# Optimization experiments

Hardware: AMD Instinct MI355X
Metric: run time of the kernel (lower is better)

The kernel has to match this reference:

```python
import jax, jax.numpy as jnp
import numpy as np

D = 1024      # model_dim
H = 16        # num_heads
DH = D // H   # depth per head
F = 4096      # ffn_dim
B, L = 4, 2048
LN_EPS = 1e-5


def layer_norm(x, g, b):
    mu = jnp.mean(x, axis=-1, keepdims=True)
    var = jnp.var(x, axis=-1, keepdims=True)
    return (x - mu) * jax.lax.rsqrt(var + LN_EPS) * g + b


def setup_inputs() -> dict:
    key = jax.random.key(0)
    ks = jax.random.split(key, 12)
    s = 0.02
    return {
        "inputs": jax.random.normal(ks[0], (B, L, D), jnp.float32),
        "Wq": jax.random.normal(ks[1], (D, D), jnp.float32) * s,
        "Wk": jax.random.normal(ks[2], (D, D), jnp.float32) * s,
        "Wv": jax.random.normal(ks[3], (D, D), jnp.float32) * s,
        "Wo": jax.random.normal(ks[4], (D, D), jnp.float32) * s,
        "W1": jax.random.normal(ks[5], (F, D), jnp.float32) * s,
        "b1": jnp.zeros((F,), jnp.float32),
        "W2": jax.random.normal(ks[6], (D, F), jnp.float32) * s,
        "b2": jnp.zeros((D,), jnp.float32),
        "ln_g": jnp.ones((D,), jnp.float32),
        "ln_b": jnp.zeros((D,), jnp.float32),
    }


def reference(inputs, Wq, Wk, Wv, Wo, W1, b1, W2, b2, ln_g, ln_b):
    # --- MultiHeadAttention (faithful to source, incl. the bug where
    # ScaledDotProductAttention returns v, not attention @ v) ---
    scale = DH ** -0.5
    q = (inputs @ Wq.T) * scale            # [B,L,D], scaled before head split
    k = inputs @ Wk.T                      # [B,L,D]
    v = inputs @ Wv.T                      # [B,L,D]
    # only the LAST head's attention scores survive the python loop
    qH = q[..., (H - 1) * DH:]             # [B,L,DH]
    kH = k[..., (H - 1) * DH:]             # [B,L,DH]
    attn = jax.nn.softmax(jnp.einsum('bqd,bkd->bqk', qH, kH), axis=-1) / H
    # combine_heads(split_heads(v)) == v, so context = Wo applied to v
    context = v @ Wo.T                     # [B,L,D]; dropout(p=0) is identity

    # --- PositionalWiseFeedForward: conv1d(kernel=1) == pointwise linear ---
    h = jax.nn.relu(context @ W1.T + b1)   # [B,L,F]
    ffn = h @ W2.T + b2                    # [B,L,D]
    out = layer_norm(context + ffn, ln_g, ln_b)
    return out, attn
```

## Files before the change

### kernel.cpp

```cpp
#include <hip/hip_runtime.h>
#include <hip/hip_bf16.h>
#include <stdint.h>

#define D_ 1024
#define H_ 16
#define DH_ 64
#define F_ 4096
#define B_ 4
#define L_ 2048
#define MTOK 8192

typedef __attribute__((ext_vector_type(8))) short bf16x8;
typedef __attribute__((ext_vector_type(4))) float f32x4;

__device__ __forceinline__ short f2bf(float f) {
  uint32_t u = __float_as_uint(f);
  uint32_t r = (u + 0x7FFFu + ((u >> 16) & 1u)) >> 16;
  return (short)(uint16_t)r;
}
__device__ __forceinline__ float bf2f(short s) {
  return __uint_as_float(((uint32_t)(uint16_t)s) << 16);
}

__device__ __forceinline__ void gload_lds16(const short* g, short* l) {
  __builtin_amdgcn_global_load_lds(
      (const __attribute__((address_space(1))) void*)g,
      (__attribute__((address_space(3))) void*)l,
      16, 0, 0);
}

__global__ void __launch_bounds__(256) convert_bf16(
    const float* __restrict__ src, short* __restrict__ dst, long n, float scale) {
  long i = ((long)blockIdx.x * 256 + threadIdx.x) * 4;
  long stride = (long)gridDim.x * 1024;
  for (; i < n; i += stride) {
    float4 f = *(const float4*)(src + i);
    short4 o;
    o.x = f2bf(f.x * scale);
    o.y = f2bf(f.y * scale);
    o.z = f2bf(f.z * scale);
    o.w = f2bf(f.w * scale);
    *(short4*)(dst + i) = o;
  }
}

__global__ void __launch_bounds__(256) convert_weights(
    const float* __restrict__ Wq, const float* __restrict__ Wk,
    const float* __restrict__ Wv, const float* __restrict__ Wo,
    const float* __restrict__ W1, const float* __restrict__ W2,
    short* __restrict__ wqk, short* __restrict__ wv, short* __restrict__ wo,
    short* __restrict__ w1, short* __restrict__ w2) {
  long i = ((long)blockIdx.x * 256 + threadIdx.x) * 4;
  const float* src; short* dst; long off; float scale = 1.0f;
  if (i < 65536L)            { src = Wq + 960L * 1024; dst = wqk;        off = i;            scale = 0.125f; }
  else if (i < 131072L)      { src = Wk + 960L * 1024; dst = wqk + 65536; off = i - 65536L;  }
  else if (i < 1179648L)     { src = Wv; dst = wv; off = i - 131072L;   }
  else if (i < 2228224L)     { src = Wo; dst = wo; off = i - 1179648L;  }
  else if (i < 6422528L)     { src = W1; dst = w1; off = i - 2228224L;  }
  else                       { src = W2; dst = w2; off = i - 6422528L;  }
  float4 f = *(const float4*)(src + off);
  short4 o4;
  o4.x = f2bf(f.x * scale); o4.y = f2bf(f.y * scale);
  o4.z = f2bf(f.z * scale); o4.w = f2bf(f.w * scale);
  *(short4*)(dst + off) = o4;
}

#define BAR   __builtin_amdgcn_s_barrier()
#define PRIO1 __builtin_amdgcn_s_setprio(1)
#define PRIO0 __builtin_amdgcn_s_setprio(0)
#define LGKM0 asm volatile("s_waitcnt lgkmcnt(0)" ::: "memory")

#define RD_A(mh_, par_) do {                                                  \
  const short* bp = lds + (par_) * BUF + wm * ASLOT;                          \
  _Pragma("unroll")                                                           \
  for (int m2 = 0; m2 < MH; m2++) {                                           \
    const int r = ((mh_) * MH + m2) * 16 + l15;                               \
    _Pragma("unroll")                                                         \
    for (int ks = 0; ks < 2; ks++)                                            \
      aF[mh_][m2][ks] =                                                       \
          *(const bf16x8*)(bp + r * 64 + (((ks * 4 + l4) ^ (r & 7)) << 3));   \
  } } while (0)

#define RD_B(nh_, par_) do {                                                  \
  const short* bp = lds + (par_) * BUF + BM * 64 + (wn >> 1) * 8192;          \
  _Pragma("unroll")                                                           \
  for (int n2 = 0; n2 < 2; n2++) {                                            \
    const int r = (wn & 1) * 64 + ((nh_) * 2 + n2) * 16 + l15;                \
    _Pragma("unroll")                                                         \
    for (int ks = 0; ks < 2; ks++)                                            \
      bF[nh_][n2][ks] =                                                       \
          *(const bf16x8*)(bp + r * 64 + (((ks * 4 + l4) ^ (r & 7)) << 3));   \
  } } while (0)

#define QUAD(mh_, nh_) do {                                                   \
  _Pragma("unroll")                                                           \
  for (int ks = 0; ks < 2; ks++)                                              \
    _Pragma("unroll")                                                         \
    for (int m2 = 0; m2 < MH; m2++)                                           \
      _Pragma("unroll")                                                       \
      for (int n2 = 0; n2 < 2; n2++)                                          \
        acc[(mh_) * MH + m2][(nh_) * 2 + n2] =                                \
            __builtin_amdgcn_mfma_f32_16x16x32_bf16(                          \
                aF[mh_][m2][ks], bF[nh_][n2][ks],                             \
                acc[(mh_) * MH + m2][(nh_) * 2 + n2], 0, 0, 0);               \
} while (0)

#define ITER2(g_, par_, SN, SPP, GK) do {                                     \
                                                                 \
  RD_A(0, par_); RD_B(0, par_); RD_B(1, par_);                                \
  if (SN) stA((g_) + 1, 1, (par_) ^ 1);                                       \
  LGKM0;                                                                      \
  PRIO1; QUAD(0, 0); QUAD(0, 1); PRIO0;                                       \
  BAR;              \
                                                                 \
  RD_A(1, par_);                                                              \
  if (SPP) { stB((g_) + 2, 0, par_); stB((g_) + 2, 1, par_);                  \
             stA((g_) + 2, 0, par_); }                                        \
  LGKM0;                                                                      \
  PRIO1; QUAD(1, 0); QUAD(1, 1); PRIO0;                                       \
  if (GK == 1) asm volatile("s_waitcnt vmcnt(%0)" :: "i"(VG) : "memory");     \
  else if (GK == 2) asm volatile("s_waitcnt vmcnt(0)" ::: "memory");          \
  BAR;                          \
} while (0)

template<int BMT, bool BIAS, bool RELU>
__global__ void __launch_bounds__(512, 2) gemm8p(
    const short* __restrict__ A, int lda,
    const short* __restrict__ Bm, int ldb,
    short* __restrict__ C, int ldc,
    const float* __restrict__ bias, int K) {
  constexpr int BM = BMT * 128;
  constexpr int MT = BMT * 4;
  constexpr int MH = MT / 2;
  constexpr int LA = BMT;
  constexpr int LB = 2;
  constexpr int ASLOT = (BM / 2) * 64;
  constexpr int BUF = BM * 64 + 16384;
  constexpr int VG = 2 * LB + LA;

  __shared__ __align__(16) short lds[2 * BUF];

  const int tid = threadIdx.x;
  const int lane = tid & 63;
  const int wave = tid >> 6;
  const int wm = wave >> 2, wn = wave & 3;
  const int l15 = lane & 15, l4 = lane >> 4;

  const int id = blockIdx.y * gridDim.x + blockIdx.x;
  const int per = (gridDim.x * gridDim.y) >> 3;
  const int swz = (id & 7) * per + (id >> 3);
  const int bn = swz % gridDim.x;
  const int bm = swz / gridDim.x;

  const short* Ab = A + (long)bm * BM * lda;
  const short* Bb = Bm + (long)bn * 256 * ldb;
  const int NTILE = K >> 6;

  const short* gA[2][LA]; short* dA[2][LA];
  const short* gB[2][LB]; short* dB[2][LB];
#pragma unroll
  for (int h = 0; h < 2; h++) {
#pragma unroll
    for (int l = 0; l < LA; l++) {
      int c = l * 512 + tid, r = c >> 3, cg = (c & 7) ^ (r & 7);
      gA[h][l] = Ab + (long)(h * (BM / 2) + r) * lda + cg * 8;
      dA[h][l] = lds + h * ASLOT + c * 8;
    }
#pragma unroll
    for (int l = 0; l < LB; l++) {
      int c = l * 512 + tid, r = c >> 3, cg = (c & 7) ^ (r & 7);
      gB[h][l] = Bb + (long)(h * 128 + r) * ldb + cg * 8;
      dB[h][l] = lds + BM * 64 + h * 8192 + c * 8;
    }
  }
  auto stA = [&](int t, int h, int par) {
#pragma unroll
    for (int l = 0; l < LA; l++)
      gload_lds16(gA[h][l] + (t << 6), dA[h][l] + par * BUF);
  };
  auto stB = [&](int t, int h, int par) {
#pragma unroll
    for (int l = 0; l < LB; l++)
      gload_lds16(gB[h][l] + (t << 6), dB[h][l] + par * BUF);
  };

  f32x4 acc[MT][4];
#pragma unroll
  for (int i = 0; i < MT; i++)
#pragma unroll
    for (int j = 0; j < 4; j++) acc[i][j] = (f32x4){0.f, 0.f, 0.f, 0.f};

  bf16x8 aF[2][MH][2];
  bf16x8 bF[2][2][2];

  stA(0, 0, 0); stA(0, 1, 0); stB(0, 0, 0); stB(0, 1, 0);
  stB(1, 0, 1); stB(1, 1, 1); stA(1, 0, 1);
  asm volatile("s_waitcnt vmcnt(%0)" :: "i"(VG) : "memory");
  BAR;

  for (int g = 0; g + 3 < NTILE; g += 2) {
    ITER2(g, 0, 1, 1, 1);
    ITER2(g + 1, 1, 1, 1, 1);
  }
  ITER2(NTILE - 2, 0, 1, 0, 2);
  ITER2(NTILE - 1, 1, 0, 0, 0);

  const int col0 = bn * 256 + wn * 64;
  const int row0 = bm * BM + wm * (BM / 2);
#pragma unroll
  for (int nt = 0; nt < 4; nt++) {
    const int col = col0 + nt * 16 + l15;
    const float bb = BIAS ? bias[col] : 0.f;
#pragma unroll
    for (int mt = 0; mt < MT; mt++) {
      const int rbase = row0 + mt * 16 + l4 * 4;
#pragma unroll
      for (int r = 0; r < 4; r++) {
        float v = acc[mt][nt][r] + bb;
        if (RELU) v = v > 0.f ? v : 0.f;
        C[(long)(rbase + r) * ldc + col] = f2bf(v);
      }
    }
  }
}

__global__ void __launch_bounds__(256) gemm_bt(
    const short* __restrict__ A, int lda,
    const short* __restrict__ Bm, int ldb,
    short* __restrict__ C, int ldc, int K) {
  const int bn = blockIdx.x;
  const int bm = blockIdx.y;
  const short* Ab = A + (long)bm * 128 * lda;
  const short* Bb = Bm + (long)bn * 128 * ldb;

  __shared__ short lA[128 * 64];
  __shared__ short lB[128 * 64];

  const int tid = threadIdx.x;
  const int lane = tid & 63;
  const int wave = tid >> 6;
  const int wr = wave >> 1, wc = wave & 1;

  f32x4 acc[4][4];
#pragma unroll
  for (int i = 0; i < 4; i++)
#pragma unroll
    for (int j = 0; j < 4; j++) acc[i][j] = (f32x4){0.f, 0.f, 0.f, 0.f};

  for (int k0 = 0; k0 < K; k0 += 64) {
    __syncthreads();
#pragma unroll
    for (int i = 0; i < 4; i++) {
      int c = i * 256 + tid;
      int row = c >> 3;
      int col = (c & 7) * 8;
      gload_lds16(Ab + (long)row * lda + k0 + col, &lA[c * 8]);
      gload_lds16(Bb + (long)row * ldb + k0 + col, &lB[c * 8]);
    }
    __syncthreads();

#pragma unroll
    for (int ks = 0; ks < 2; ks++) {
      bf16x8 af[4], bfr[4];
#pragma unroll
      for (int t = 0; t < 4; t++) {
        af[t]  = *(const bf16x8*)&lA[(wr * 64 + t * 16 + (lane & 15)) * 64 + ks * 32 + (lane >> 4) * 8];
        bfr[t] = *(const bf16x8*)&lB[(wc * 64 + t * 16 + (lane & 15)) * 64 + ks * 32 + (lane >> 4) * 8];
      }
#pragma unroll
      for (int mt = 0; mt < 4; mt++)
#pragma unroll
        for (int nt = 0; nt < 4; nt++)
          acc[mt][nt] = __builtin_amdgcn_mfma_f32_16x16x32_bf16(af[mt], bfr[nt], acc[mt][nt], 0, 0, 0);
    }
  }

  const int col0 = bn * 128 + wc * 64;
  const int row0 = bm * 128 + wr * 64;
#pragma unroll
  for (int mt = 0; mt < 4; mt++) {
#pragma unroll
    for (int nt = 0; nt < 4; nt++) {
      int col = col0 + nt * 16 + (lane & 15);
      int rbase = row0 + mt * 16 + (lane >> 4) * 4;
#pragma unroll
      for (int r = 0; r < 4; r++)
        C[(long)(rbase + r) * ldc + col] = f2bf(acc[mt][nt][r]);
    }
  }
}

__global__ void __launch_bounds__(256) fused_attn(
    const short* __restrict__ qkh, float* __restrict__ attn) {
  const int tid = threadIdx.x;
  const int lane = tid & 63;
  const int wave = tid >> 6;
  const int grp = wave >> 1;
  const int half = wave & 1;
  const int l15 = lane & 15, l4 = lane >> 4;
  const int b = blockIdx.y;
  const int q0 = blockIdx.x * 32 + grp * 16;
  const long base = (long)b * 2048;

  bf16x8 qf[2];
#pragma unroll
  for (int ks = 0; ks < 2; ks++)
    qf[ks] = *(const bf16x8*)&qkh[(base + q0 + l15) * 128 + ks * 32 + l4 * 8];

  const short* kb = qkh + (base + (long)half * 1024) * 128 + 64;

  float m = -1e30f, s = 0.f;
  for (int kt = 0; kt < 64; kt++) {
    bf16x8 kf0 = *(const bf16x8*)&kb[(kt * 16 + l15) * 128 + l4 * 8];
    bf16x8 kf1 = *(const bf16x8*)&kb[(kt * 16 + l15) * 128 + 32 + l4 * 8];
    f32x4 acc = (f32x4){0.f, 0.f, 0.f, 0.f};
    acc = __builtin_amdgcn_mfma_f32_16x16x32_bf16(kf0, qf[0], acc, 0, 0, 0);
    acc = __builtin_amdgcn_mfma_f32_16x16x32_bf16(kf1, qf[1], acc, 0, 0, 0);
    float pm = fmaxf(fmaxf(acc[0], acc[1]), fmaxf(acc[2], acc[3]));
    float mn = fmaxf(m, pm);
    s = s * __expf(m - mn) + __expf(acc[0] - mn) + __expf(acc[1] - mn) +
        __expf(acc[2] - mn) + __expf(acc[3] - mn);
    m = mn;
  }
#pragma unroll
  for (int o = 16; o <= 32; o <<= 1) {
    float m2 = __shfl_xor(m, o, 64);
    float s2 = __shfl_xor(s, o, 64);
    float mn = fmaxf(m, m2);
    s = s * __expf(m - mn) + s2 * __expf(m2 - mn);
    m = mn;
  }
  __shared__ float lm[2][2][16], lsm[2][2][16];
  if (lane < 16) { lm[grp][half][lane] = m; lsm[grp][half][lane] = s; }
  __syncthreads();
  {
    float m0 = lm[grp][0][l15], m1 = lm[grp][1][l15];
    float s0 = lsm[grp][0][l15], s1 = lsm[grp][1][l15];
    float M = fmaxf(m0, m1);
    s = s0 * __expf(m0 - M) + s1 * __expf(m1 - M);
    m = M;
  }
  const float inv = 1.0f / (s * 16.0f);

  __shared__ float tb[4][256];
  float* attb = attn + (base + q0) * 2048 + half * 1024;
  for (int kt = 0; kt < 64; kt++) {
    bf16x8 kf0 = *(const bf16x8*)&kb[(kt * 16 + l15) * 128 + l4 * 8];
    bf16x8 kf1 = *(const bf16x8*)&kb[(kt * 16 + l15) * 128 + 32 + l4 * 8];
    f32x4 acc = (f32x4){0.f, 0.f, 0.f, 0.f};
    acc = __builtin_amdgcn_mfma_f32_16x16x32_bf16(kf0, qf[0], acc, 0, 0, 0);
    acc = __builtin_amdgcn_mfma_f32_16x16x32_bf16(kf1, qf[1], acc, 0, 0, 0);
    f32x4 p;
#pragma unroll
    for (int r = 0; r < 4; r++) p[r] = __expf(acc[r] - m) * inv;
    *(f32x4*)&tb[wave][l15 * 16 + l4 * 4] = p;
#pragma unroll
    for (int rr = 0; rr < 4; rr++) {
      int row = rr * 4 + l4;
      attb[(long)row * 2048 + kt * 16 + l15] = tb[wave][row * 16 + l15];
    }
  }
}

__device__ __forceinline__ float wave_sum(float v) {
#pragma unroll
  for (int o = 32; o > 0; o >>= 1) v += __shfl_xor(v, o, 64);
  return v;
}

__global__ void __launch_bounds__(256) ln_fuse(
    const short* __restrict__ ctx, const short* __restrict__ ffn,
    const float* __restrict__ g, const float* __restrict__ bta,
    float* __restrict__ out) {
  const int tid = threadIdx.x;
  long base = (long)blockIdx.x * 1024 + tid * 4;
  short4 c4 = *(const short4*)(ctx + base);
  short4 f4 = *(const short4*)(ffn + base);
  float x0 = bf2f(c4.x) + bf2f(f4.x);
  float x1 = bf2f(c4.y) + bf2f(f4.y);
  float x2 = bf2f(c4.z) + bf2f(f4.z);
  float x3 = bf2f(c4.w) + bf2f(f4.w);

  float s = (x0 + x1) + (x2 + x3);
  float q = (x0 * x0 + x1 * x1) + (x2 * x2 + x3 * x3);
  __shared__ float rs[4], rq[4];
  s = wave_sum(s);
  q = wave_sum(q);
  if ((tid & 63) == 0) { rs[tid >> 6] = s; rq[tid >> 6] = q; }
  __syncthreads();
  float S = rs[0] + rs[1] + rs[2] + rs[3];
  float Q = rq[0] + rq[1] + rq[2] + rq[3];
  float mu = S * (1.0f / 1024.0f);
  float var = Q * (1.0f / 1024.0f) - mu * mu;
  float inv = rsqrtf(var + 1e-5f);

  float4 g4 = *(const float4*)(g + tid * 4);
  float4 b4 = *(const float4*)(bta + tid * 4);
  float4 o;
  o.x = (x0 - mu) * inv * g4.x + b4.x;
  o.y = (x1 - mu) * inv * g4.y + b4.y;
  o.z = (x2 - mu) * inv * g4.z + b4.z;
  o.w = (x3 - mu) * inv * g4.w + b4.w;
  *(float4*)(out + base) = o;
}

extern "C" void kernel_launch(void* const* d_in, const int* in_sizes, int n_in,
                              void* d_out, int out_size, void* d_ws, size_t ws_size,
                              hipStream_t stream) {
  const float* inputs = (const float*)d_in[0];
  const float* Wq = (const float*)d_in[1];
  const float* Wk = (const float*)d_in[2];
  const float* Wv = (const float*)d_in[3];
  const float* Wo = (const float*)d_in[4];
  const float* W1 = (const float*)d_in[5];
  const float* b1 = (const float*)d_in[6];
  const float* W2 = (const float*)d_in[7];
  const float* b2 = (const float*)d_in[8];
  const float* ln_g = (const float*)d_in[9];
  const float* ln_b = (const float*)d_in[10];

  char* w = (char*)d_ws;
  short* in_bf = (short*)w;  w += (long)MTOK * D_ * 2;
  short* wqk   = (short*)w;  w += 128L * D_ * 2;
  short* wv    = (short*)w;  w += (long)D_ * D_ * 2;
  short* wo    = (short*)w;  w += (long)D_ * D_ * 2;
  short* w1    = (short*)w;  w += (long)F_ * D_ * 2;
  short* w2    = (short*)w;  w += (long)D_ * F_ * 2;
  short* qkh   = (short*)w;  w += (long)MTOK * 128 * 2;
  short* vbf   = (short*)w;  w += (long)MTOK * D_ * 2;
  short* ctxbf = (short*)w;  w += (long)MTOK * D_ * 2;
  short* hbf   = (short*)w;  w += (long)MTOK * F_ * 2;
  short* ffnbf = (short*)w;  w += (long)MTOK * D_ * 2;

  float* out  = (float*)d_out;
  float* attn = out + (long)MTOK * D_;

  convert_bf16<<<dim3((MTOK * D_) >> 10), 256, 0, stream>>>(
      inputs, in_bf, (long)MTOK * D_, 1.0f);
  convert_weights<<<dim3(10368), 256, 0, stream>>>(
      Wq, Wk, Wv, Wo, W1, W2, wqk, wv, wo, w1, w2);

  gemm_bt<<<dim3(1, 64), 256, 0, stream>>>(in_bf, D_, wqk, D_, qkh, 128, D_);
  fused_attn<<<dim3(64, 4), 256, 0, stream>>>(qkh, attn);
  gemm8p<1, false, false><<<dim3(4, 64), 512, 0, stream>>>(
      in_bf, D_, wv, D_, vbf, D_, nullptr, D_);
  gemm8p<1, false, false><<<dim3(4, 64), 512, 0, stream>>>(
      vbf, D_, wo, D_, ctxbf, D_, nullptr, D_);
  gemm8p<2, true, true><<<dim3(16, 32), 512, 0, stream>>>(
      ctxbf, D_, w1, D_, hbf, F_, b1, D_);
  gemm8p<1, true, false><<<dim3(4, 64), 512, 0, stream>>>(
      hbf, F_, w2, F_, ffnbf, D_, b2, F_);
  ln_fuse<<<dim3(MTOK), 256, 0, stream>>>(ctxbf, ffnbf, ln_g, ln_b, out);
}
```

Measured before the change: 298.1 us.

## Fold Wo into Wv and restructure attention softmax to single-pass register scores

Precomputes the fused weight Wo·Wv with a bf16 transpose plus a small GEMM, so the per-token V and output projections become one 8192x1024x1024 GEMM instead of two. The attention kernel now spreads each 16-query block across 8 waves, each owning 256 keys. Each wave keeps its scores in registers, computes max and sum in one pass, and writes fp32 probabilities directly as vectorized row stores, removing the second QK recompute and the LDS transpose. The risks are an extra bf16 rounding of the fused weight, which changes numerics slightly, and higher register pressure in the attention kernel.

```diff
diff --git a/kernel.cpp b/kernel.cpp
--- a/kernel.cpp
+++ b/kernel.cpp
@@ -65,6 +65,29 @@
   *(short4*)(dst + off) = o4;
 }
 
+__global__ void __launch_bounds__(256) transpose_bf16_1k(
+    const short* __restrict__ src, short* __restrict__ dst) {
+  __shared__ short t[64][65];
+  const int bx = blockIdx.x, by = blockIdx.y;
+  const int lr = threadIdx.x >> 4;
+  const int lc = (threadIdx.x & 15) * 4;
+#pragma unroll
+  for (int rr = 0; rr < 4; rr++) {
+    int r = lr * 4 + rr;
+    short4 v = *(const short4*)&src[(long)(by * 64 + r) * 1024 + bx * 64 + lc];
+    t[r][lc] = v.x; t[r][lc + 1] = v.y; t[r][lc + 2] = v.z; t[r][lc + 3] = v.w;
+  }
+  __syncthreads();
+#pragma unroll
+  for (int rr = 0; rr < 4; rr++) {
+    int r = lr * 4 + rr;
+    short4 v;
+    v.x = t[lc + 0][r]; v.y = t[lc + 1][r];
+    v.z = t[lc + 2][r]; v.w = t[lc + 3][r];
+    *(short4*)&dst[(long)(bx * 64 + r) * 1024 + by * 64 + lc] = v;
+  }
+}
+
 #define BAR   __builtin_amdgcn_s_barrier()
 #define PRIO1 __builtin_amdgcn_s_setprio(1)
 #define PRIO0 __builtin_amdgcn_s_setprio(0)
@@ -290,16 +313,14 @@
   }
 }
 
-__global__ void __launch_bounds__(256) fused_attn(
+__global__ void __launch_bounds__(512) fused_attn(
     const short* __restrict__ qkh, float* __restrict__ attn) {
   const int tid = threadIdx.x;
   const int lane = tid & 63;
   const int wave = tid >> 6;
-  const int grp = wave >> 1;
-  const int half = wave & 1;
   const int l15 = lane & 15, l4 = lane >> 4;
   const int b = blockIdx.y;
-  const int q0 = blockIdx.x * 32 + grp * 16;
+  const int q0 = blockIdx.x * 16;
   const long base = (long)b * 2048;
 
   bf16x8 qf[2];
@@ -307,58 +328,56 @@
   for (int ks = 0; ks < 2; ks++)
     qf[ks] = *(const bf16x8*)&qkh[(base + q0 + l15) * 128 + ks * 32 + l4 * 8];
 
-  const short* kb = qkh + (base + (long)half * 1024) * 128 + 64;
-
-  float m = -1e30f, s = 0.f;
-  for (int kt = 0; kt < 64; kt++) {
+  const short* kb = qkh + (base + (long)wave * 256) * 128 + 64;
+
+  f32x4 s[16];
+#pragma unroll
+  for (int kt = 0; kt < 16; kt++) {
     bf16x8 kf0 = *(const bf16x8*)&kb[(kt * 16 + l15) * 128 + l4 * 8];
     bf16x8 kf1 = *(const bf16x8*)&kb[(kt * 16 + l15) * 128 + 32 + l4 * 8];
-    f32x4 acc = (f32x4){0.f, 0.f, 0.f, 0.f};
-    acc = __builtin_amdgcn_mfma_f32_16x16x32_bf16(kf0, qf[0], acc, 0, 0, 0);
-    acc = __builtin_amdgcn_mfma_f32_16x16x32_bf16(kf1, qf[1], acc, 0, 0, 0);
-    float pm = fmaxf(fmaxf(acc[0], acc[1]), fmaxf(acc[2], acc[3]));
-    float mn = fmaxf(m, pm);
-    s = s * __expf(m - mn) + __expf(acc[0] - mn) + __expf(acc[1] - mn) +
-        __expf(acc[2] - mn) + __expf(acc[3] - mn);
-    m = mn;
-  }
-#pragma unroll
-  for (int o = 16; o <= 32; o <<= 1) {
-    float m2 = __shfl_xor(m, o, 64);
-    float s2 = __shfl_xor(s, o, 64);
-    float mn = fmaxf(m, m2);
-    s = s * __expf(m - mn) + s2 * __expf(m2 - mn);
-    m = mn;
-  }
-  __shared__ float lm[2][2][16], lsm[2][2][16];
-  if (lane < 16) { lm[grp][half][lane] = m; lsm[grp][half][lane] = s; }
+    f32x4 a = (f32x4){0.f, 0.f, 0.f, 0.f};
+    a = __builtin_amdgcn_mfma_f32_16x16x32_bf16(kf0, qf[0], a, 0, 0, 0);
+    a = __builtin_amdgcn_mfma_f32_16x16x32_bf16(kf1, qf[1], a, 0, 0, 0);
+    s[kt] = a;
+  }
+
+  float m = -1e30f;
+#pragma unroll
+  for (int kt = 0; kt < 16; kt++)
+    m = fmaxf(m, fmaxf(fmaxf(s[kt][0], s[kt][1]), fmaxf(s[kt][2], s[kt][3])));
+#pragma unroll
+  for (int o = 16; o <= 32; o <<= 1) m = fmaxf(m, __shfl_xor(m, o, 64));
+
+  float ss = 0.f;
+#pragma unroll
+  for (int kt = 0; kt < 16; kt++) {
+    f32x4 e;
+#pragma unroll
+    for (int r = 0; r < 4; r++) e[r] = __expf(s[kt][r] - m);
+    s[kt] = e;
+    ss += (e[0] + e[1]) + (e[2] + e[3]);
+  }
+#pragma unroll
+  for (int o = 16; o <= 32; o <<= 1) ss += __shfl_xor(ss, o, 64);
+
+  __shared__ float lm[8][16], lsm[8][16];
+  if (lane < 16) { lm[wave][l15] = m; lsm[wave][l15] = ss; }
   __syncthreads();
-  {
-    float m0 = lm[grp][0][l15], m1 = lm[grp][1][l15];
-    float s0 = lsm[grp][0][l15], s1 = lsm[grp][1][l15];
-    float M = fmaxf(m0, m1);
-    s = s0 * __expf(m0 - M) + s1 * __expf(m1 - M);
-    m = M;
-  }
-  const float inv = 1.0f / (s * 16.0f);
-
-  __shared__ float tb[4][256];
-  float* attb = attn + (base + q0) * 2048 + half * 1024;
-  for (int kt = 0; kt < 64; kt++) {
-    bf16x8 kf0 = *(const bf16x8*)&kb[(kt * 16 + l15) * 128 + l4 * 8];
-    bf16x8 kf1 = *(const bf16x8*)&kb[(kt * 16 + l15) * 128 + 32 + l4 * 8];
-    f32x4 acc = (f32x4){0.f, 0.f, 0.f, 0.f};
-    acc = __builtin_amdgcn_mfma_f32_16x16x32_bf16(kf0, qf[0], acc, 0, 0, 0);
-    acc = __builtin_amdgcn_mfma_f32_16x16x32_bf16(kf1, qf[1], acc, 0, 0, 0);
+  float M = -1e30f;
+#pragma unroll
+  for (int w2 = 0; w2 < 8; w2++) M = fmaxf(M, lm[w2][l15]);
+  float S = 0.f;
+#pragma unroll
+  for (int w2 = 0; w2 < 8; w2++) S += lsm[w2][l15] * __expf(lm[w2][l15] - M);
+  const float f = __expf(m - M) / (S * 16.0f);
+
+  float* attb = attn + (base + q0 + l15) * 2048 + wave * 256 + l4 * 4;
+#pragma unroll
+  for (int kt = 0; kt < 16; kt++) {
     f32x4 p;
 #pragma unroll
-    for (int r = 0; r < 4; r++) p[r] = __expf(acc[r] - m) * inv;
-    *(f32x4*)&tb[wave][l15 * 16 + l4 * 4] = p;
-#pragma unroll
-    for (int rr = 0; rr < 4; rr++) {
-      int row = rr * 4 + l4;
-      attb[(long)row * 2048 + kt * 16 + l15] = tb[wave][row * 16 + l15];
-    }
+    for (int r = 0; r < 4; r++) p[r] = s[kt][r] * f;
+    *(f32x4*)(attb + kt * 16) = p;
   }
 }
 
@@ -427,7 +446,8 @@
   short* w1    = (short*)w;  w += (long)F_ * D_ * 2;
   short* w2    = (short*)w;  w += (long)D_ * F_ * 2;
   short* qkh   = (short*)w;  w += (long)MTOK * 128 * 2;
-  short* vbf   = (short*)w;  w += (long)MTOK * D_ * 2;
+  short* wvT   = (short*)w;  w += (long)D_ * D_ * 2;
+  short* wf    = (short*)w;  w += (long)D_ * D_ * 2;
   short* ctxbf = (short*)w;  w += (long)MTOK * D_ * 2;
   short* hbf   = (short*)w;  w += (long)MTOK * F_ * 2;
   short* ffnbf = (short*)w;  w += (long)MTOK * D_ * 2;
@@ -440,12 +460,13 @@
   convert_weights<<<dim3(10368), 256, 0, stream>>>(
       Wq, Wk, Wv, Wo, W1, W2, wqk, wv, wo, w1, w2);
 
+  transpose_bf16_1k<<<dim3(16, 16), 256, 0, stream>>>(wv, wvT);
+  gemm_bt<<<dim3(8, 8), 256, 0, stream>>>(wo, D_, wvT, D_, wf, D_, D_);
+
   gemm_bt<<<dim3(1, 64), 256, 0, stream>>>(in_bf, D_, wqk, D_, qkh, 128, D_);
-  fused_attn<<<dim3(64, 4), 256, 0, stream>>>(qkh, attn);
+  fused_attn<<<dim3(128, 4), 512, 0, stream>>>(qkh, attn);
   gemm8p<1, false, false><<<dim3(4, 64), 512, 0, stream>>>(
-      in_bf, D_, wv, D_, vbf, D_, nullptr, D_);
-  gemm8p<1, false, false><<<dim3(4, 64), 512, 0, stream>>>(
-      vbf, D_, wo, D_, ctxbf, D_, nullptr, D_);
+      in_bf, D_, wf, D_, ctxbf, D_, nullptr, D_);
   gemm8p<2, true, true><<<dim3(16, 32), 512, 0, stream>>>(
       ctxbf, D_, w1, D_, hbf, F_, b1, D_);
   gemm8p<1, true, false><<<dim3(4, 64), 512, 0, stream>>>(
```

Result: faster. 275.2 us (-7.7%).
